# Performance work log

Measured on AMD Instinct MI355X. Metric: run time of the kernel, lower is better.

Reference implementation:

```python
import jax, jax.numpy as jnp
import numpy as np
from jax import lax

D_MODEL = 1024
D_FF = 4096
NUM_EXPERTS = 24
TOP_K = 2
B, S = 2, 2048


def setup_inputs() -> dict:
    key = jax.random.key(0)
    ks = jax.random.split(key, 5)
    x = jax.random.normal(ks[0], (B, S, D_MODEL), dtype=jnp.float32)
    gate_w = jax.random.normal(ks[1], (D_MODEL, NUM_EXPERTS), dtype=jnp.float32) * 0.02
    gate_b = jnp.zeros((NUM_EXPERTS,), dtype=jnp.float32)
    w1 = jax.random.normal(ks[2], (NUM_EXPERTS, D_MODEL, D_FF), dtype=jnp.float32) * 0.02
    b1 = jnp.zeros((NUM_EXPERTS, D_FF), dtype=jnp.float32)
    w2 = jax.random.normal(ks[3], (NUM_EXPERTS, D_FF, D_MODEL), dtype=jnp.float32) * 0.02
    b2 = jnp.zeros((NUM_EXPERTS, D_MODEL), dtype=jnp.float32)
    return {"x": x, "gate_w": gate_w, "gate_b": gate_b,
            "w1": w1, "b1": b1, "w2": w2, "b2": b2}


def reference(x, gate_w, gate_b, w1, b1, w2, b2):
    b, s, d = x.shape
    t = b * s
    xf = x.reshape(t, d)  # [T, d]
    scores = xf @ gate_w + gate_b  # [T, E]
    top_val, top_idx = lax.top_k(scores, TOP_K)  # [T, k]
    prob = jax.nn.softmax(top_val, axis=-1)  # softmax over the top-k logits
    # scatter top-k probabilities into dense per-expert combine weights [T, E]
    combine = jnp.zeros((t, NUM_EXPERTS), dtype=x.dtype)
    combine = combine.at[jnp.arange(t)[:, None], top_idx].add(prob)

    def body(acc, expert):
        w1e, b1e, w2e, b2e, ce = expert  # ce: [T]
        h = jax.nn.gelu(xf @ w1e + b1e, approximate=False)  # exact GELU as torch default
        y = h @ w2e + b2e  # [T, d]
        return acc + ce[:, None] * y, None

    out, _ = lax.scan(body, jnp.zeros_like(xf), (w1, b1, w2, b2, combine.T))
    return out.reshape(b, s, d)
```

## Files before the change

### kernel.cpp

```cpp
#include <hip/hip_runtime.h>
#include <math.h>

#define DM 1024
#define DF 4096
#define NE 24
#define T_TOK 4096
#define T2 (T_TOK*2)

#define BM 128
#define BN 128
#define BK 64
#define NK1 (DM / BK)
#define NK2H (DF / BK / 2)
#define NTMAX 88

typedef __attribute__((ext_vector_type(4))) float f32x4;
typedef __attribute__((ext_vector_type(2))) float f32x2;
typedef __attribute__((ext_vector_type(8))) short s16x8;

static __device__ __forceinline__ unsigned short f2bf(float f) {
    unsigned int u = __float_as_uint(f);
    unsigned int r = u + 0x7fffu + ((u >> 16) & 1u);
    return (unsigned short)(r >> 16);
}

static __device__ __forceinline__ unsigned int cvtpk(float lo, float hi) {
    unsigned int r;
    asm("v_cvt_pk_bf16_f32 %0, %1, %2" : "=v"(r) : "v"(lo), "v"(hi));
    return r;
}

#define GLL(gsrc, ldst)                                                          \
    __builtin_amdgcn_global_load_lds(                                            \
        (const __attribute__((address_space(1))) void*)(gsrc),                   \
        (__attribute__((address_space(3))) void*)(ldst), 16, 0, 0)


__global__ void k_transpose_gw(const float* __restrict__ gw, float* __restrict__ gwT) {
    int e = blockIdx.x;
    for (int d = threadIdx.x; d < DM; d += blockDim.x)
        gwT[e * DM + d] = gw[d * NE + e];
}

__global__ void k_gate(const float* __restrict__ x, const float* __restrict__ gwT,
                       const float* __restrict__ gb,
                       int* __restrict__ idx, float* __restrict__ prob) {
    int wave = threadIdx.x >> 6;
    int lane = threadIdx.x & 63;
    int t = blockIdx.x * 4 + wave;
    if (t >= T_TOK) return;
    const float* xr = x + (size_t)t * DM;
    float acc[NE];
#pragma unroll
    for (int e = 0; e < NE; e++) acc[e] = 0.f;
    for (int i = 0; i < DM / 64; i++) {
        int d = lane + i * 64;
        float xv = xr[d];
#pragma unroll
        for (int e = 0; e < NE; e++) acc[e] = fmaf(xv, gwT[e * DM + d], acc[e]);
    }
#pragma unroll
    for (int e = 0; e < NE; e++) {
        float v = acc[e];
        for (int off = 32; off >= 1; off >>= 1) v += __shfl_xor(v, off);
        acc[e] = v;
    }
    if (lane == 0) {
        float v1 = -1e30f, v2 = -1e30f;
        int i1 = -1, i2 = -1;
        for (int e = 0; e < NE; e++) {
            float s = acc[e] + gb[e];
            if (s > v1) { v2 = v1; i2 = i1; v1 = s; i1 = e; }
            else if (s > v2) { v2 = s; i2 = e; }
        }
        float e2 = expf(v2 - v1);
        float inv = 1.f / (1.f + e2);
        idx[t * 2] = i1; idx[t * 2 + 1] = i2;
        prob[t * 2] = inv; prob[t * 2 + 1] = e2 * inv;
    }
}


__global__ __launch_bounds__(1024)
void k_route(const int* __restrict__ idx, int* __restrict__ counts,
             int* __restrict__ offsets, int* __restrict__ slot_tok,
             int* __restrict__ pair_slot, int* __restrict__ tmap,
             int* __restrict__ ntiles) {
    __shared__ int cnt[NE], offs[NE], cur[NE];
    const int tid = threadIdx.x;
    if (tid < NE) cnt[tid] = 0;
    __syncthreads();
    for (int i = tid; i < T2; i += 1024) atomicAdd(&cnt[idx[i]], 1);
    __syncthreads();
    if (tid == 0) {
        int s = 0, nt = 0;
        for (int e = 0; e < NE; e++) {
            offs[e] = s; offsets[e] = s; counts[e] = cnt[e]; s += cnt[e];
            for (int mt = 0; mt * BM < cnt[e]; mt++) tmap[nt++] = (e << 8) | mt;
        }
        ntiles[0] = nt;
    }
    if (tid < NE) cur[tid] = 0;
    __syncthreads();
    for (int i = tid; i < T2; i += 1024) {
        int e = idx[i];
        int pos = offs[e] + atomicAdd(&cur[e], 1);
        slot_tok[pos] = i >> 1;
        pair_slot[i] = pos;
    }
}

__global__ void k_gather(const float* __restrict__ x, const int* __restrict__ slot_tok,
                         unsigned short* __restrict__ Xg) {
    int s = blockIdx.x;
    int tok = slot_tok[s];
    const float4* src = (const float4*)(x + (size_t)tok * DM);
    ushort4* dst = (ushort4*)(Xg + (size_t)s * DM);
    for (int i = threadIdx.x; i < DM / 4; i += blockDim.x) {
        float4 v = src[i];
        ushort4 o;
        o.x = f2bf(v.x); o.y = f2bf(v.y); o.z = f2bf(v.z); o.w = f2bf(v.w);
        dst[i] = o;
    }
}

__global__ void k_combine(const float* __restrict__ Y1, const float* __restrict__ Y2,
                          const int* __restrict__ pair_slot,
                          const float* __restrict__ prob, const int* __restrict__ idx,
                          const float* __restrict__ b2, float* __restrict__ out) {
    int t = blockIdx.x;
    int s1 = pair_slot[t * 2], s2 = pair_slot[t * 2 + 1];
    int e1 = idx[t * 2], e2 = idx[t * 2 + 1];
    float p1 = prob[t * 2], p2 = prob[t * 2 + 1];
    const float4* y1a = (const float4*)(Y1 + (size_t)s1 * DM);
    const float4* y1b = (const float4*)(Y2 + (size_t)s1 * DM);
    const float4* y2a = (const float4*)(Y1 + (size_t)s2 * DM);
    const float4* y2b = (const float4*)(Y2 + (size_t)s2 * DM);
    const float4* ba = (const float4*)(b2 + (size_t)e1 * DM);
    const float4* bb = (const float4*)(b2 + (size_t)e2 * DM);
    float4* o = (float4*)(out + (size_t)t * DM);
    int i = threadIdx.x;
    float4 a0 = y1a[i], a1 = y1b[i], b0 = y2a[i], b1 = y2b[i];
    float4 c = ba[i], d = bb[i];
    float4 r;
    r.x = p1 * (a0.x + a1.x + c.x) + p2 * (b0.x + b1.x + d.x);
    r.y = p1 * (a0.y + a1.y + c.y) + p2 * (b0.y + b1.y + d.y);
    r.z = p1 * (a0.z + a1.z + c.z) + p2 * (b0.z + b1.z + d.z);
    r.w = p1 * (a0.w + a1.w + c.w) + p2 * (b0.w + b1.w + d.w);
    o[i] = r;
}


__global__ __launch_bounds__(512)
void k_mm1(const unsigned short* __restrict__ Xg, const float* __restrict__ w1,
           const float* __restrict__ b1, const int* __restrict__ counts,
           const int* __restrict__ offsets, const int* __restrict__ tmap,
           const int* __restrict__ ntiles, unsigned short* __restrict__ H) {
    const int TOT = NTMAX * 32;
    int work = (blockIdx.x & 7) * (TOT >> 3) + (blockIdx.x >> 3);
    const int ti = work % NTMAX;
    if (ti >= ntiles[0]) return;
    const int n0 = (work / NTMAX) * BN;
    const int tm = tmap[ti];
    const int e = tm >> 8, mt = tm & 255;
    const int ne = counts[e];
    const int m0 = mt * BM;
    const int rows = min(BM, ne - m0);
    const int slotbase = offsets[e] + m0;

    __shared__ unsigned short As[2][BM * BK];
    __shared__ unsigned short Bs[BN * BK];

    const int tid  = threadIdx.x;
    const int lane = tid & 63;
    const int w    = tid >> 6;
    const int wm   = w >> 1, wn = w & 1;

    const float* w1e = w1 + (size_t)e * DM * DF;
    const int arow = lane >> 3;
    const int gchunk = ((lane & 7) ^ arow) * 8;

    const int swz0 = ((lane >> 4) ^ (lane & 7)) << 4;
    const int swz1 = ((4 | (lane >> 4)) ^ (lane & 7)) << 4;
    const char* Arow0 = (const char*)As[0] + (wm * 32 + (lane & 15)) * 128;
    const char* Arow1 = (const char*)As[1] + (wm * 32 + (lane & 15)) * 128;
    const char* Brow  = (const char*)Bs + (wn * 64 + (lane & 15)) * 128;

    const int np = (tid & 63) * 2;
    const int ckw = w;
    char* BsW0 = (char*)Bs + (np + 0) * 128 + ((ckw ^ ((np + 0) & 7)) << 4);
    char* BsW1 = (char*)Bs + (np + 1) * 128 + ((ckw ^ ((np + 1) & 7)) << 4);

    f32x4 acc[2][4];
#pragma unroll
    for (int a = 0; a < 2; a++)
#pragma unroll
        for (int b = 0; b < 4; b++) acc[a][b] = (f32x4)0.f;

    f32x2 L[8];
    auto loadB = [&](int k0) {
#pragma unroll
        for (int j = 0; j < 8; j++)
            L[j] = *(const f32x2*)(w1e + (size_t)(k0 + w * 8 + j) * DF + n0 + np);
    };
    auto stageA = [&](int buf, int k0) {
#pragma unroll
        for (int q = 0; q < 2; q++) {
            int row = (w * 2 + q) * 8 + arow;
            GLL(Xg + (size_t)(slotbase + row) * DM + k0 + gchunk,
                &As[buf][(w * 2 + q) * 512]);
        }
    };

    stageA(0, 0);
    loadB(0);
#pragma unroll 1
    for (int kt = 0; kt < NK1; ++kt) {
        const int cur = kt & 1;
        __syncthreads();
        if (kt + 1 < NK1) stageA(cur ^ 1, (kt + 1) * BK);
        {
            uint4 v0, v1;
            v0.x = cvtpk(L[0][0], L[1][0]);
            v0.y = cvtpk(L[2][0], L[3][0]);
            v0.z = cvtpk(L[4][0], L[5][0]);
            v0.w = cvtpk(L[6][0], L[7][0]);
            v1.x = cvtpk(L[0][1], L[1][1]);
            v1.y = cvtpk(L[2][1], L[3][1]);
            v1.z = cvtpk(L[4][1], L[5][1]);
            v1.w = cvtpk(L[6][1], L[7][1]);
            *(uint4*)BsW0 = v0;
            *(uint4*)BsW1 = v1;
        }
        if (kt + 1 < NK1) loadB((kt + 1) * BK);
        const char* Arow = cur ? Arow1 : Arow0;
        s16x8 af[2][2];
#pragma unroll
        for (int f = 0; f < 2; f++) {
            af[0][f] = *(const s16x8*)(Arow + f * 2048 + swz0);
            af[1][f] = *(const s16x8*)(Arow + f * 2048 + swz1);
        }
        asm volatile("s_waitcnt lgkmcnt(0)" ::: "memory");
        __builtin_amdgcn_s_barrier();
        __builtin_amdgcn_sched_barrier(0);
        s16x8 bfr[2][4];
#pragma unroll
        for (int f = 0; f < 4; f++) {
            bfr[0][f] = *(const s16x8*)(Brow + f * 2048 + swz0);
            bfr[1][f] = *(const s16x8*)(Brow + f * 2048 + swz1);
        }
#pragma unroll
        for (int ks = 0; ks < 2; ks++)
#pragma unroll
            for (int fm = 0; fm < 2; fm++)
#pragma unroll
                for (int fn = 0; fn < 4; fn++)
                    acc[fm][fn] = __builtin_amdgcn_mfma_f32_16x16x32_bf16(
                        af[ks][fm], bfr[ks][fn], acc[fm][fn], 0, 0, 0);
    }

    const float* b1e = b1 + (size_t)e * DF;
#pragma unroll
    for (int fm = 0; fm < 2; fm++) {
        const int mrow = wm * 32 + fm * 16 + ((lane >> 4) << 2);
#pragma unroll
        for (int fn = 0; fn < 4; fn++) {
            const int ncol = n0 + wn * 64 + fn * 16 + (lane & 15);
            const float bb = b1e[ncol];
#pragma unroll
            for (int r = 0; r < 4; r++) {
                const int m = mrow + r;
                if (m < rows) {
                    float h = acc[fm][fn][r] + bb;
                    h = 0.5f * h * (1.f + erff(h * 0.70710678118654752f));
                    H[(size_t)(slotbase + m) * DF + ncol] = f2bf(h);
                }
            }
        }
    }
}

__global__ __launch_bounds__(512)
void k_mm2(const unsigned short* __restrict__ Hb, const float* __restrict__ w2,
           const int* __restrict__ counts, const int* __restrict__ offsets,
           const int* __restrict__ tmap, const int* __restrict__ ntiles,
           float* __restrict__ Y1, float* __restrict__ Y2) {
    const int TOT = NTMAX * 16;
    int work = (blockIdx.x & 7) * (TOT >> 3) + (blockIdx.x >> 3);
    const int ti = work % NTMAX;
    if (ti >= ntiles[0]) return;
    const int r2 = work / NTMAX;
    const int ksl = r2 & 1;
    const int n0 = (r2 >> 1) * BN;
    const int tm = tmap[ti];
    const int e = tm >> 8, mt = tm & 255;
    const int ne = counts[e];
    const int m0 = mt * BM;
    const int rows = min(BM, ne - m0);
    const int slotbase = offsets[e] + m0;
    const int kbeg = ksl * (DF / 2);
    float* Y = ksl ? Y2 : Y1;

    __shared__ unsigned short As[2][BM * BK];
    __shared__ unsigned short Bs[BN * BK];

    const int tid  = threadIdx.x;
    const int lane = tid & 63;
    const int w    = tid >> 6;
    const int wm   = w >> 1, wn = w & 1;

    const float* w2e = w2 + (size_t)e * DF * DM;
    const int arow = lane >> 3;
    const int gchunk = ((lane & 7) ^ arow) * 8;

    const int swz0 = ((lane >> 4) ^ (lane & 7)) << 4;
    const int swz1 = ((4 | (lane >> 4)) ^ (lane & 7)) << 4;
    const char* Arow0 = (const char*)As[0] + (wm * 32 + (lane & 15)) * 128;
    const char* Arow1 = (const char*)As[1] + (wm * 32 + (lane & 15)) * 128;
    const char* Brow  = (const char*)Bs + (wn * 64 + (lane & 15)) * 128;

    const int np = (tid & 63) * 2;
    const int ckw = w;
    char* BsW0 = (char*)Bs + (np + 0) * 128 + ((ckw ^ ((np + 0) & 7)) << 4);
    char* BsW1 = (char*)Bs + (np + 1) * 128 + ((ckw ^ ((np + 1) & 7)) << 4);

    f32x4 acc[2][4];
#pragma unroll
    for (int a = 0; a < 2; a++)
#pragma unroll
        for (int b = 0; b < 4; b++) acc[a][b] = (f32x4)0.f;

    f32x2 L[8];
    auto loadB = [&](int k0) {
#pragma unroll
        for (int j = 0; j < 8; j++)
            L[j] = *(const f32x2*)(w2e + (size_t)(k0 + w * 8 + j) * DM + n0 + np);
    };
    auto stageA = [&](int buf, int k0) {
#pragma unroll
        for (int q = 0; q < 2; q++) {
            int row = (w * 2 + q) * 8 + arow;
            GLL(Hb + (size_t)(slotbase + row) * DF + k0 + gchunk,
                &As[buf][(w * 2 + q) * 512]);
        }
    };

    stageA(0, kbeg);
    loadB(kbeg);
#pragma unroll 1
    for (int kt = 0; kt < NK2H; ++kt) {
        const int cur = kt & 1;
        __syncthreads();
        if (kt + 1 < NK2H) stageA(cur ^ 1, kbeg + (kt + 1) * BK);
        {
            uint4 v0, v1;
            v0.x = cvtpk(L[0][0], L[1][0]);
            v0.y = cvtpk(L[2][0], L[3][0]);
            v0.z = cvtpk(L[4][0], L[5][0]);
            v0.w = cvtpk(L[6][0], L[7][0]);
            v1.x = cvtpk(L[0][1], L[1][1]);
            v1.y = cvtpk(L[2][1], L[3][1]);
            v1.z = cvtpk(L[4][1], L[5][1]);
            v1.w = cvtpk(L[6][1], L[7][1]);
            *(uint4*)BsW0 = v0;
            *(uint4*)BsW1 = v1;
        }
        if (kt + 1 < NK2H) loadB(kbeg + (kt + 1) * BK);
        const char* Arow = cur ? Arow1 : Arow0;
        s16x8 af[2][2];
#pragma unroll
        for (int f = 0; f < 2; f++) {
            af[0][f] = *(const s16x8*)(Arow + f * 2048 + swz0);
            af[1][f] = *(const s16x8*)(Arow + f * 2048 + swz1);
        }
        asm volatile("s_waitcnt lgkmcnt(0)" ::: "memory");
        __builtin_amdgcn_s_barrier();
        __builtin_amdgcn_sched_barrier(0);
        s16x8 bfr[2][4];
#pragma unroll
        for (int f = 0; f < 4; f++) {
            bfr[0][f] = *(const s16x8*)(Brow + f * 2048 + swz0);
            bfr[1][f] = *(const s16x8*)(Brow + f * 2048 + swz1);
        }
#pragma unroll
        for (int ks = 0; ks < 2; ks++)
#pragma unroll
            for (int fm = 0; fm < 2; fm++)
#pragma unroll
                for (int fn = 0; fn < 4; fn++)
                    acc[fm][fn] = __builtin_amdgcn_mfma_f32_16x16x32_bf16(
                        af[ks][fm], bfr[ks][fn], acc[fm][fn], 0, 0, 0);
    }

#pragma unroll
    for (int fm = 0; fm < 2; fm++) {
        const int mrow = wm * 32 + fm * 16 + ((lane >> 4) << 2);
#pragma unroll
        for (int fn = 0; fn < 4; fn++) {
            const int ncol = n0 + wn * 64 + fn * 16 + (lane & 15);
#pragma unroll
            for (int r = 0; r < 4; r++) {
                const int m = mrow + r;
                if (m < rows)
                    Y[(size_t)(slotbase + m) * DM + ncol] = acc[fm][fn][r];
            }
        }
    }
}


extern "C" void kernel_launch(void* const* d_in, const int* in_sizes, int n_in,
                              void* d_out, int out_size, void* d_ws, size_t ws_size,
                              hipStream_t stream) {
    const float* x   = (const float*)d_in[0];
    const float* gw  = (const float*)d_in[1];
    const float* gb  = (const float*)d_in[2];
    const float* w1  = (const float*)d_in[3];
    const float* b1  = (const float*)d_in[4];
    const float* w2  = (const float*)d_in[5];
    const float* b2  = (const float*)d_in[6];
    float* out = (float*)d_out;

    size_t off = 0;
    auto alloc = [&](size_t bytes) {
        void* p = (char*)d_ws + off;
        off += (bytes + 255) & ~(size_t)255;
        return p;
    };
    float* gwT       = (float*)alloc(NE * DM * sizeof(float));
    int*   idx       = (int*)alloc(T2 * sizeof(int));
    float* prob      = (float*)alloc(T2 * sizeof(float));
    int*   counts    = (int*)alloc(32 * sizeof(int));
    int*   offsets   = (int*)alloc(32 * sizeof(int));
    int*   slot_tok  = (int*)alloc(T2 * sizeof(int));
    int*   pair_slot = (int*)alloc(T2 * sizeof(int));
    int*   tmap      = (int*)alloc(128 * sizeof(int));
    int*   ntiles    = (int*)alloc(32 * sizeof(int));
    unsigned short* Xg = (unsigned short*)alloc((size_t)(T2 + BM) * DM * sizeof(unsigned short));
    unsigned short* Hb = (unsigned short*)alloc((size_t)(T2 + BM) * DF * sizeof(unsigned short));
    float* Yb        = (float*)alloc((size_t)(T2 + BM) * DM * sizeof(float));
    float* Yb2       = (float*)alloc((size_t)(T2 + BM) * DM * sizeof(float));

    k_transpose_gw<<<NE, 256, 0, stream>>>(gw, gwT);
    k_gate<<<T_TOK / 4, 256, 0, stream>>>(x, gwT, gb, idx, prob);
    k_route<<<1, 1024, 0, stream>>>(idx, counts, offsets, slot_tok, pair_slot, tmap, ntiles);
    k_gather<<<T2, 256, 0, stream>>>(x, slot_tok, Xg);

    k_mm1<<<NTMAX * 32, 512, 0, stream>>>(Xg, w1, b1, counts, offsets, tmap, ntiles, Hb);
    k_mm2<<<NTMAX * 16, 512, 0, stream>>>(Hb, w2, counts, offsets, tmap, ntiles, Yb, Yb2);
    k_combine<<<T_TOK, 256, 0, stream>>>(Yb, Yb2, pair_slot, prob, idx, b2, out);
}
```

Before: 466.2 us.

## Deepen B-operand register prefetch to two stages with explicit vmcnt waits

Both expert GEMM kernels now keep two register buffers of fp32 weight tiles and load the weights two k-steps ahead instead of one. The k-loop is unrolled by two to alternate between the buffers. The __syncthreads is replaced by an explicit s_waitcnt vmcnt plus s_barrier so the newer loads can stay in flight. The aim is to hide global weight-load latency behind more MFMA work, at the cost of more registers and fragile hand-counted vmcnt accounting.

New measurement: 538.4 us. 15.5% more time.

```diff
diff --git a/kernel.cpp b/kernel.cpp
--- a/kernel.cpp
+++ b/kernel.cpp
@@ -197,8 +197,8 @@
 #pragma unroll
         for (int b = 0; b < 4; b++) acc[a][b] = (f32x4)0.f;
 
-    f32x2 L[8];
-    auto loadB = [&](int k0) {
+    f32x2 LA[8], LB[8];
+    auto loadBt = [&](f32x2 (&L)[8], int k0) {
 #pragma unroll
         for (int j = 0; j < 8; j++)
             L[j] = *(const f32x2*)(w1e + (size_t)(k0 + w * 8 + j) * DF + n0 + np);
@@ -211,14 +211,11 @@
                 &As[buf][(w * 2 + q) * 512]);
         }
     };
-
-    stageA(0, 0);
-    loadB(0);
-#pragma unroll 1
-    for (int kt = 0; kt < NK1; ++kt) {
-        const int cur = kt & 1;
-        __syncthreads();
-        if (kt + 1 < NK1) stageA(cur ^ 1, (kt + 1) * BK);
+    auto stepk = [&](int kt, f32x2 (&L)[8], const char* Arow, int nbuf) {
+        if (kt + 1 < NK1) asm volatile("s_waitcnt vmcnt(8)" ::: "memory");
+        else              asm volatile("s_waitcnt vmcnt(0)" ::: "memory");
+        __builtin_amdgcn_s_barrier();
+        __builtin_amdgcn_sched_barrier(0);
         {
             uint4 v0, v1;
             v0.x = cvtpk(L[0][0], L[1][0]);
@@ -232,8 +229,8 @@
             *(uint4*)BsW0 = v0;
             *(uint4*)BsW1 = v1;
         }
-        if (kt + 1 < NK1) loadB((kt + 1) * BK);
-        const char* Arow = cur ? Arow1 : Arow0;
+        if (kt + 1 < NK1) stageA(nbuf, (kt + 1) * BK);
+        if (kt + 2 < NK1) loadBt(L, (kt + 2) * BK);
         s16x8 af[2][2];
 #pragma unroll
         for (int f = 0; f < 2; f++) {
@@ -257,6 +254,15 @@
                 for (int fn = 0; fn < 4; fn++)
                     acc[fm][fn] = __builtin_amdgcn_mfma_f32_16x16x32_bf16(
                         af[ks][fm], bfr[ks][fn], acc[fm][fn], 0, 0, 0);
+    };
+
+    stageA(0, 0);
+    loadBt(LA, 0);
+    loadBt(LB, BK);
+#pragma unroll 1
+    for (int kt2 = 0; kt2 < NK1; kt2 += 2) {
+        stepk(kt2,     LA, (kt2 & 1) ? Arow1 : Arow0, 1);
+        stepk(kt2 + 1, LB, Arow1, 0);
     }
 
     const float* b1e = b1 + (size_t)e * DF;
@@ -330,8 +336,8 @@
 #pragma unroll
         for (int b = 0; b < 4; b++) acc[a][b] = (f32x4)0.f;
 
-    f32x2 L[8];
-    auto loadB = [&](int k0) {
+    f32x2 LA[8], LB[8];
+    auto loadBt = [&](f32x2 (&L)[8], int k0) {
 #pragma unroll
         for (int j = 0; j < 8; j++)
             L[j] = *(const f32x2*)(w2e + (size_t)(k0 + w * 8 + j) * DM + n0 + np);
@@ -344,14 +350,11 @@
                 &As[buf][(w * 2 + q) * 512]);
         }
     };
-
-    stageA(0, kbeg);
-    loadB(kbeg);
-#pragma unroll 1
-    for (int kt = 0; kt < NK2H; ++kt) {
-        const int cur = kt & 1;
-        __syncthreads();
-        if (kt + 1 < NK2H) stageA(cur ^ 1, kbeg + (kt + 1) * BK);
+    auto stepk = [&](int kt, f32x2 (&L)[8], const char* Arow, int nbuf) {
+        if (kt + 1 < NK2H) asm volatile("s_waitcnt vmcnt(8)" ::: "memory");
+        else               asm volatile("s_waitcnt vmcnt(0)" ::: "memory");
+        __builtin_amdgcn_s_barrier();
+        __builtin_amdgcn_sched_barrier(0);
         {
             uint4 v0, v1;
             v0.x = cvtpk(L[0][0], L[1][0]);
@@ -365,8 +368,8 @@
             *(uint4*)BsW0 = v0;
             *(uint4*)BsW1 = v1;
         }
-        if (kt + 1 < NK2H) loadB(kbeg + (kt + 1) * BK);
-        const char* Arow = cur ? Arow1 : Arow0;
+        if (kt + 1 < NK2H) stageA(nbuf, kbeg + (kt + 1) * BK);
+        if (kt + 2 < NK2H) loadBt(L, kbeg + (kt + 2) * BK);
         s16x8 af[2][2];
 #pragma unroll
         for (int f = 0; f < 2; f++) {
@@ -390,6 +393,15 @@
                 for (int fn = 0; fn < 4; fn++)
                     acc[fm][fn] = __builtin_amdgcn_mfma_f32_16x16x32_bf16(
                         af[ks][fm], bfr[ks][fn], acc[fm][fn], 0, 0, 0);
+    };
+
+    stageA(0, kbeg);
+    loadBt(LA, kbeg);
+    loadBt(LB, kbeg + BK);
+#pragma unroll 1
+    for (int kt2 = 0; kt2 < NK2H; kt2 += 2) {
+        stepk(kt2,     LA, (kt2 & 1) ? Arow1 : Arow0, 1);
+        stepk(kt2 + 1, LB, Arow1, 0);
     }
 
 #pragma unroll
```
